# Performance work log

Hardware: AMD Instinct MI355X
Metric: run time of the kernel (lower is better)

## Reference

```python
import jax, jax.numpy as jnp
import numpy as np

D_MODEL = 1024
EXPANSION = 4
NUM_TILES = 4
D_FF = D_MODEL * EXPANSION


def setup_inputs() -> dict:
    key = jax.random.key(0)
    k1, k2, k3, k4, k5 = jax.random.split(key, 5)
    x = jax.random.normal(k1, (8, 2048, D_MODEL), dtype=jnp.float32)
    w_up = jax.random.normal(k2, (D_FF, D_MODEL), dtype=jnp.float32) * 0.02
    b_up = jax.random.normal(k3, (D_FF,), dtype=jnp.float32) * 0.02
    w_down = jax.random.normal(k4, (D_MODEL, D_FF), dtype=jnp.float32) * 0.02
    b_down = jax.random.normal(k5, (D_MODEL,), dtype=jnp.float32) * 0.02
    return {"x": x, "w_up": w_up, "b_up": b_up, "w_down": w_down, "b_down": b_down}


def reference(x, w_up, b_up, w_down, b_down):
    B, T, C = x.shape
    xf = x.reshape(B * T, C)  # [N, d_model]
    N = B * T

    # Emergent tile signatures: sign of per-tile row sums of up_proj weight.
    tile_up = D_FF // NUM_TILES
    signatures = jnp.sign(w_up.reshape(NUM_TILES, tile_up, C).sum(axis=1))  # [num_tiles, d_model]

    # Routing: argmax over input-signature alignment -> one-hot gate.
    scores = xf @ signatures.T                      # [N, num_tiles]
    winner = jnp.argmax(scores, axis=-1)            # [N]
    gate = jax.nn.one_hot(winner, NUM_TILES, dtype=xf.dtype)  # [N, num_tiles]

    # Tile-gated up projection (gate scales output tile blocks), then ReLU.
    hidden = xf @ w_up.T + b_up                     # [N, d_ff]
    hidden = (hidden.reshape(N, NUM_TILES, tile_up) * gate[:, :, None]).reshape(N, D_FF)
    hidden = jax.nn.relu(hidden)

    # Tile-gated down projection.
    tile_down = D_MODEL // NUM_TILES
    out = hidden @ w_down.T + b_down                # [N, d_model]
    out = (out.reshape(N, NUM_TILES, tile_down) * gate[:, :, None]).reshape(N, D_MODEL)

    return out.reshape(B, T, D_MODEL), gate.reshape(B, T, NUM_TILES)
```

## Files before the change

kernel.cpp:

```cpp
#include <hip/hip_runtime.h>
#include <stdint.h>
#include <stddef.h>

#define N_TOK 16384
#define DM    1024
#define DFF   4096
#define NT    4
#define TU    1024
#define TD    256

typedef __attribute__((ext_vector_type(8))) short  short8;
typedef __attribute__((ext_vector_type(4))) short  short4v;
typedef __attribute__((ext_vector_type(4))) float  floatx4;

__device__ inline unsigned short f2bf(float f){
  union { float f; uint32_t u; } v; v.f = f;
  uint32_t u = v.u + 0x7FFFu + ((v.u >> 16) & 1u);
  return (unsigned short)(u >> 16);
}

__device__ __forceinline__ void gll16(const void* g, void* l){
  __builtin_amdgcn_global_load_lds(
      (const __attribute__((address_space(1))) unsigned int*)g,
      (__attribute__((address_space(3))) unsigned int*)l,
      16, 0, 0);
}

__global__ void k_sig_partial(const float* __restrict__ w_up,
                              float* __restrict__ partial,
                              unsigned short* __restrict__ wupb){
  const int b = blockIdx.x, tid = threadIdx.x;
  const int tile = b >> 6, chunk = b & 63;
  const int c0 = tid * 4;
  const int row0 = tile*TU + chunk*16;
  float s0=0.f, s1=0.f, s2=0.f, s3=0.f;
  const float* base = w_up + (size_t)row0 * DM + c0;
  #pragma unroll
  for (int r = 0; r < 16; ++r){
    floatx4 v = *(const floatx4*)(base + (size_t)r * DM);
    s0 += v[0]; s1 += v[1]; s2 += v[2]; s3 += v[3];
    short4v p;
    p[0]=(short)f2bf(v[0]); p[1]=(short)f2bf(v[1]);
    p[2]=(short)f2bf(v[2]); p[3]=(short)f2bf(v[3]);
    *(short4v*)(wupb + (size_t)(row0 + r) * DM + c0) = p;
  }
  float* p = partial + ((size_t)tile*DM + c0) * 64 + chunk;
  p[0] = s0; p[64] = s1; p[128] = s2; p[192] = s3;
}

__global__ void k_sig_final(const float* __restrict__ partial,
                            float* __restrict__ sig){
  const int g = blockIdx.x * 256 + threadIdx.x;
  const float* p = partial + (size_t)g * 64;
  float s = 0.f;
  #pragma unroll
  for (int i = 0; i < 64; ++i) s += p[i];
  sig[g] = (s > 0.f) ? 1.f : ((s < 0.f) ? -1.f : 0.f);
}

__global__ void k_wdown_conv(const float* __restrict__ w,
                             unsigned short* __restrict__ wb){
  const size_t i = ((size_t)blockIdx.x * 256 + threadIdx.x) * 8;
  floatx4 v0 = *(const floatx4*)(w + i);
  floatx4 v1 = *(const floatx4*)(w + i + 4);
  short8 p;
  p[0]=(short)f2bf(v0[0]); p[1]=(short)f2bf(v0[1]); p[2]=(short)f2bf(v0[2]); p[3]=(short)f2bf(v0[3]);
  p[4]=(short)f2bf(v1[0]); p[5]=(short)f2bf(v1[1]); p[6]=(short)f2bf(v1[2]); p[7]=(short)f2bf(v1[3]);
  *(short8*)(wb + i) = p;
}

__global__ __launch_bounds__(256) void k_route(
    const float* __restrict__ x, const float* __restrict__ sig,
    float* __restrict__ gate_out, int* __restrict__ winner,
    unsigned short* __restrict__ xbf){
  __shared__ float ssig[NT * DM];
  const int tid = threadIdx.x;
  for (int i = tid; i < NT*DM; i += 256) ssig[i] = sig[i];
  __syncthreads();
  const int wv = tid >> 6, lane = tid & 63;
  const int n = blockIdx.x * 4 + wv;
  const float* xr = x + (size_t)n * DM;
  unsigned short* xb = xbf + (size_t)n * 2048 + 1024;
  double a0=0.0, a1=0.0, a2=0.0, a3=0.0;
  #pragma unroll
  for (int j = 0; j < 4; ++j){
    const int c = j*256 + lane*4;
    floatx4 v = *(const floatx4*)(xr + c);
    short4v p;
    p[0]=(short)f2bf(v[0]); p[1]=(short)f2bf(v[1]);
    p[2]=(short)f2bf(v[2]); p[3]=(short)f2bf(v[3]);
    *(short4v*)(xb + c) = p;
    #pragma unroll
    for (int u = 0; u < 4; ++u){
      double xv = (double)v[u];
      a0 += xv * (double)ssig[c+u];
      a1 += xv * (double)ssig[DM   + c+u];
      a2 += xv * (double)ssig[2*DM + c+u];
      a3 += xv * (double)ssig[3*DM + c+u];
    }
  }
  #pragma unroll
  for (int off = 32; off > 0; off >>= 1){
    a0 += __shfl_down(a0, off, 64);
    a1 += __shfl_down(a1, off, 64);
    a2 += __shfl_down(a2, off, 64);
    a3 += __shfl_down(a3, off, 64);
  }
  if (lane == 0){
    double s[4] = {a0, a1, a2, a3};
    int w = 0;
    #pragma unroll
    for (int t = 1; t < 4; ++t) if (s[t] > s[w]) w = t;
    floatx4 g = { w==0 ? 1.f:0.f, w==1 ? 1.f:0.f, w==2 ? 1.f:0.f, w==3 ? 1.f:0.f };
    *(floatx4*)(gate_out + (size_t)n * 4) = g;
    winner[n] = w;
  }
}

__global__ void k_hist(const int* __restrict__ winner,
                       int* __restrict__ blk_cnt){
  __shared__ int wcnt[4][NT];
  const int tid = threadIdx.x, wv = tid >> 6, lane = tid & 63;
  const int w = winner[blockIdx.x * 256 + tid];
  #pragma unroll
  for (int t = 0; t < NT; ++t){
    unsigned long long m = __ballot(w == t);
    if (lane == 0) wcnt[wv][t] = __popcll(m);
  }
  __syncthreads();
  if (tid < NT){
    int s = wcnt[0][tid] + wcnt[1][tid] + wcnt[2][tid] + wcnt[3][tid];
    blk_cnt[blockIdx.x * NT + tid] = s;
  }
}

__global__ void k_scan(const int* __restrict__ blk_cnt,
                       int* __restrict__ meta, int* __restrict__ blk_base){
  __shared__ int s[256];
  const int tid = threadIdx.x;
  s[tid] = blk_cnt[tid];
  __syncthreads();
  if (tid == 0){
    int tot[NT] = {0,0,0,0};
    for (int b = 0; b < 64; ++b)
      for (int t = 0; t < NT; ++t) tot[t] += s[b*NT + t];
    int off = 0, base[NT];
    for (int t = 0; t < NT; ++t){ meta[t] = tot[t]; meta[4+t] = off; base[t] = off; off += tot[t]; }
    for (int b = 0; b < 64; ++b)
      for (int t = 0; t < NT; ++t){ int c = s[b*NT + t]; s[b*NT + t] = base[t]; base[t] += c; }
  }
  __syncthreads();
  blk_base[tid] = s[tid];
}

__global__ void k_scatter(const int* __restrict__ winner,
                          const int* __restrict__ blk_base,
                          int* __restrict__ idx){
  __shared__ int wcnt[4][NT];
  const int tid = threadIdx.x, wv = tid >> 6, lane = tid & 63;
  const int n = blockIdx.x * 256 + tid;
  const int w = winner[n];
  unsigned long long mymask = 0;
  #pragma unroll
  for (int t = 0; t < NT; ++t){
    unsigned long long m = __ballot(w == t);
    if (lane == 0) wcnt[wv][t] = __popcll(m);
    if (t == w) mymask = m;
  }
  __syncthreads();
  const unsigned long long below = (lane == 0) ? 0ull : (~0ull >> (64 - lane));
  int pos = blk_base[blockIdx.x * NT + w] + __popcll(mymask & below);
  for (int v = 0; v < wv; ++v) pos += wcnt[v][w];
  idx[pos] = n;
}

__global__ __launch_bounds__(256, 2) void k_gemm1(
    const unsigned short* __restrict__ xbf,
    const unsigned short* __restrict__ wupb,
    const float* __restrict__ b_up, const int* __restrict__ meta,
    const int* __restrict__ idx, unsigned short* __restrict__ hid){
  const int tile = blockIdx.z;
  const int cnt  = meta[tile];
  const int p0   = blockIdx.x * 128;
  if (p0 >= cnt) return;
  const int off  = meta[4 + tile];
  const int nb   = blockIdx.y;

  __shared__ unsigned short smem[16384];
  unsigned short* As0 = smem;
  unsigned short* As1 = smem + 4096;
  unsigned short* Bs0 = smem + 8192;
  unsigned short* Bs1 = smem + 12288;
  __shared__ int nrow[128];

  const int tid = threadIdx.x;
  if (tid < 128){
    int p = p0 + tid;
    nrow[tid] = idx[off + (p < cnt ? p : cnt - 1)];
  }
  __syncthreads();

  const int wv = tid >> 6, lane = tid & 63;
  const int wm = (wv >> 1) * 64, wn = (wv & 1) * 64;
  const int l16 = lane & 15, quad = lane >> 4;

  const int rsub = lane >> 2;
  const int kus  = (lane & 3) * 8;

  const int ra = wv*32 + rsub;
  const unsigned short* aptr0 = xbf + (size_t)nrow[ra]      * 2048 + 1024 + kus;
  const unsigned short* aptr1 = xbf + (size_t)nrow[ra + 16] * 2048 + 1024 + kus;
  const unsigned short* bptr0 = wupb + (size_t)(tile*TU + nb*128 + wv*32 + rsub) * DM + kus;
  const unsigned short* bptr1 = bptr0 + 16 * DM;

  unsigned short* a0d0 = As0 + (wv*32) * 32;  unsigned short* a0d1 = a0d0 + 16*32;
  unsigned short* a1d0 = As1 + (wv*32) * 32;  unsigned short* a1d1 = a1d0 + 16*32;
  unsigned short* b0d0 = Bs0 + (wv*32) * 32;  unsigned short* b0d1 = b0d0 + 16*32;
  unsigned short* b1d0 = Bs1 + (wv*32) * 32;  unsigned short* b1d1 = b1d0 + 16*32;

  floatx4 acc[4][4];
  #pragma unroll
  for (int i = 0; i < 4; ++i)
    #pragma unroll
    for (int j = 0; j < 4; ++j) acc[i][j] = (floatx4){0.f,0.f,0.f,0.f};

  for (int k0 = 0; k0 < DM; k0 += 64){
    gll16(aptr0 + k0,      a0d0);
    gll16(aptr1 + k0,      a0d1);
    gll16(aptr0 + k0 + 32, a1d0);
    gll16(aptr1 + k0 + 32, a1d1);
    gll16(bptr0 + k0,      b0d0);
    gll16(bptr1 + k0,      b0d1);
    gll16(bptr0 + k0 + 32, b1d0);
    gll16(bptr1 + k0 + 32, b1d1);
    __syncthreads();
    {
      short8 af[4], bfr[4];
      #pragma unroll
      for (int i = 0; i < 4; ++i) af[i]  = *(const short8*)(As0 + (wm + i*16 + l16)*32 + quad*8);
      #pragma unroll
      for (int j = 0; j < 4; ++j) bfr[j] = *(const short8*)(Bs0 + (wn + j*16 + l16)*32 + quad*8);
      #pragma unroll
      for (int i = 0; i < 4; ++i)
        #pragma unroll
        for (int j = 0; j < 4; ++j)
          acc[i][j] = __builtin_amdgcn_mfma_f32_16x16x32_bf16(af[i], bfr[j], acc[i][j], 0, 0, 0);
    }
    {
      short8 af[4], bfr[4];
      #pragma unroll
      for (int i = 0; i < 4; ++i) af[i]  = *(const short8*)(As1 + (wm + i*16 + l16)*32 + quad*8);
      #pragma unroll
      for (int j = 0; j < 4; ++j) bfr[j] = *(const short8*)(Bs1 + (wn + j*16 + l16)*32 + quad*8);
      #pragma unroll
      for (int i = 0; i < 4; ++i)
        #pragma unroll
        for (int j = 0; j < 4; ++j)
          acc[i][j] = __builtin_amdgcn_mfma_f32_16x16x32_bf16(af[i], bfr[j], acc[i][j], 0, 0, 0);
    }
    __syncthreads();
  }

  const int gcol0 = nb*128;
  #pragma unroll
  for (int half = 0; half < 2; ++half){
    if ((wv >> 1) == half){
      #pragma unroll
      for (int i = 0; i < 4; ++i){
        #pragma unroll
        for (int j = 0; j < 4; ++j){
          const int col = wn + j*16 + l16;
          const float bias = b_up[tile*TU + gcol0 + col];
          #pragma unroll
          for (int r = 0; r < 4; ++r){
            const int lrow = i*16 + quad*4 + r;
            float v = acc[i][j][r] + bias;
            smem[lrow*136 + col] = f2bf(v > 0.f ? v : 0.f);
          }
        }
      }
    }
    __syncthreads();
    #pragma unroll
    for (int c = tid; c < 1024; c += 256){
      const int lrow = c >> 4, k8 = (c & 15) * 8;
      const int m = half*64 + lrow;
      if (p0 + m < cnt){
        short8 vv = *(const short8*)(smem + lrow*136 + k8);
        *(short8*)(hid + (size_t)nrow[m]*2048 + gcol0 + k8) = vv;
      }
    }
    __syncthreads();
  }
}

__global__ __launch_bounds__(256, 2) void k_gemm2(
    const unsigned short* __restrict__ hid,
    const unsigned short* __restrict__ wdownb,
    const float* __restrict__ b_down, const int* __restrict__ meta,
    const int* __restrict__ idx, float* __restrict__ out){
  const int tile = blockIdx.z;
  const int cnt  = meta[tile];
  const int p0   = blockIdx.x * 32;
  if (p0 >= cnt) return;
  const int off  = meta[4 + tile];

  __shared__ unsigned short smem[18432];
  unsigned short* As0 = smem;
  unsigned short* As1 = smem + 1024;
  unsigned short* Bs0 = smem + 2048;
  unsigned short* Bs1 = smem + 10240;
  float* epi = (float*)smem;
  __shared__ int nrow[32];

  const int tid = threadIdx.x;
  if (tid < 32){
    int p = p0 + tid;
    nrow[tid] = idx[off + (p < cnt ? p : cnt - 1)];
  }
  __syncthreads();

  const int wv = tid >> 6, lane = tid & 63;
  const int wn = wv * 64;
  const int l16 = lane & 15, quad = lane >> 4;

  const int rsub = lane >> 2;
  const int kus  = (lane & 3) * 8;

  const int arow = (wv & 1)*16 + rsub;
  const unsigned short* aptr = hid + (size_t)nrow[arow] * 2048 + kus;
  const int aoff = (wv >> 1) * 32;
  unsigned short* asd = (wv < 2 ? As0 : As1) + ((wv & 1)*16) * 32;
  const unsigned short* bptr = wdownb + (size_t)(tile*TD + wv*64 + rsub) * DFF + tile*TU + kus;
  unsigned short* bsd0 = Bs0 + (wv*64) * 32;
  unsigned short* bsd1 = Bs1 + (wv*64) * 32;

  floatx4 acc[2][4];
  #pragma unroll
  for (int i = 0; i < 2; ++i)
    #pragma unroll
    for (int j = 0; j < 4; ++j) acc[i][j] = (floatx4){0.f,0.f,0.f,0.f};

  for (int k0 = 0; k0 < TU; k0 += 64){
    gll16(aptr + k0 + aoff, asd);
    gll16(bptr + k0,               bsd0);
    gll16(bptr + k0 + 16*DFF,      bsd0 + 16*32);
    gll16(bptr + k0 + 32*DFF,      bsd0 + 32*32);
    gll16(bptr + k0 + 48*DFF,      bsd0 + 48*32);
    gll16(bptr + k0 + 32,          bsd1);
    gll16(bptr + k0 + 32 + 16*DFF, bsd1 + 16*32);
    gll16(bptr + k0 + 32 + 32*DFF, bsd1 + 32*32);
    gll16(bptr + k0 + 32 + 48*DFF, bsd1 + 48*32);
    __syncthreads();
    {
      short8 af[2], bfr[4];
      #pragma unroll
      for (int i = 0; i < 2; ++i) af[i]  = *(const short8*)(As0 + (i*16 + l16)*32 + quad*8);
      #pragma unroll
      for (int j = 0; j < 4; ++j) bfr[j] = *(const short8*)(Bs0 + (wn + j*16 + l16)*32 + quad*8);
      #pragma unroll
      for (int i = 0; i < 2; ++i)
        #pragma unroll
        for (int j = 0; j < 4; ++j)
          acc[i][j] = __builtin_amdgcn_mfma_f32_16x16x32_bf16(af[i], bfr[j], acc[i][j], 0, 0, 0);
    }
    {
      short8 af[2], bfr[4];
      #pragma unroll
      for (int i = 0; i < 2; ++i) af[i]  = *(const short8*)(As1 + (i*16 + l16)*32 + quad*8);
      #pragma unroll
      for (int j = 0; j < 4; ++j) bfr[j] = *(const short8*)(Bs1 + (wn + j*16 + l16)*32 + quad*8);
      #pragma unroll
      for (int i = 0; i < 2; ++i)
        #pragma unroll
        for (int j = 0; j < 4; ++j)
          acc[i][j] = __builtin_amdgcn_mfma_f32_16x16x32_bf16(af[i], bfr[j], acc[i][j], 0, 0, 0);
    }
    __syncthreads();
  }

  const floatx4 z4 = {0.f, 0.f, 0.f, 0.f};
  #pragma unroll
  for (int cb = 0; cb < 4; ++cb){
    if (cb == tile) continue;
    for (int c = tid; c < 32*64; c += 256){
      const int rowl = c >> 6, c4 = (c & 63) * 4;
      if (p0 + rowl < cnt)
        *(floatx4*)(out + (size_t)nrow[rowl]*DM + cb*256 + c4) = z4;
    }
  }

  #pragma unroll
  for (int half = 0; half < 2; ++half){
    #pragma unroll
    for (int j = 0; j < 4; ++j){
      const int col = wn + j*16 + l16;
      const float bias = b_down[tile*TD + col];
      #pragma unroll
      for (int r = 0; r < 4; ++r){
        const int lrow = quad*4 + r;
        epi[lrow*260 + col] = acc[half][j][r] + bias;
      }
    }
    __syncthreads();
    #pragma unroll
    for (int c = tid; c < 1024; c += 256){
      const int lrow = c >> 6, c4 = (c & 63) * 4;
      const int m = half*16 + lrow;
      if (p0 + m < cnt){
        floatx4 v = *(const floatx4*)(epi + lrow*260 + c4);
        *(floatx4*)(out + (size_t)nrow[m]*DM + tile*TD + c4) = v;
      }
    }
    __syncthreads();
  }
}

extern "C" void kernel_launch(void* const* d_in, const int* in_sizes, int n_in,
                              void* d_out, int out_size, void* d_ws, size_t ws_size,
                              hipStream_t stream){
  const float* x      = (const float*)d_in[0];
  const float* w_up   = (const float*)d_in[1];
  const float* b_up   = (const float*)d_in[2];
  const float* w_down = (const float*)d_in[3];
  const float* b_down = (const float*)d_in[4];

  unsigned short* wupb   = (unsigned short*)d_ws;
  unsigned short* wdownb = wupb + (size_t)DFF * DM;
  float* partial = (float*)(wdownb + (size_t)DM * DFF);
  float* sig     = partial + 262144;
  int*   ints    = (int*)(sig + 4096);
  int*   winner   = ints;
  int*   idx      = ints + 16384;
  int*   meta     = ints + 32768;
  int*   blk_cnt  = ints + 32776;
  int*   blk_base = ints + 33032;

  float*          out  = (float*)d_out;
  float*          gate = out + (size_t)N_TOK * DM;
  unsigned short* ob16 = (unsigned short*)d_out;

  k_sig_partial<<<dim3(NT*64), 256, 0, stream>>>(w_up, partial, wupb);
  k_sig_final  <<<dim3(16),    256, 0, stream>>>(partial, sig);
  k_wdown_conv <<<dim3(2048),  256, 0, stream>>>(w_down, wdownb);
  k_route      <<<dim3(N_TOK/4), 256, 0, stream>>>(x, sig, gate, winner, ob16);
  k_hist       <<<dim3(64),    256, 0, stream>>>(winner, blk_cnt);
  k_scan       <<<dim3(1),     256, 0, stream>>>(blk_cnt, meta, blk_base);
  k_scatter    <<<dim3(64),    256, 0, stream>>>(winner, blk_base, idx);
  k_gemm1      <<<dim3(128, 8, NT), 256, 0, stream>>>(ob16, wupb, b_up, meta, idx, ob16);
  k_gemm2      <<<dim3(512, 1, NT), 256, 0, stream>>>(ob16, wdownb, b_down, meta, idx, out);
}
```

Measured before the change: 273.5 us.

## Merge weight-conversion kernels, amortize signature loads in routing, swizzle gemm1 blocks

Merges the w_up signature/conversion kernel and the w_down bf16 conversion into one launch, removing a kernel launch and the gap between them. The routing kernel now handles 16 tokens per block and keeps the signature values in registers, so shared-memory signature reloads are amortized over four tokens per wave. The gemm1 block index is remapped so that consecutive blocks share the same row tile across the eight column blocks, which should improve L2 reuse of the gathered activations. Costs: higher register pressure in routing and fewer routing blocks.

Measured after the change: 267.1 us. -2.3%, faster.

```diff
diff --git a/kernel.cpp b/kernel.cpp
--- a/kernel.cpp
+++ b/kernel.cpp
@@ -26,10 +26,23 @@
       16, 0, 0);
 }
 
-__global__ void k_sig_partial(const float* __restrict__ w_up,
-                              float* __restrict__ partial,
-                              unsigned short* __restrict__ wupb){
-  const int b = blockIdx.x, tid = threadIdx.x;
+__global__ void k_prep(const float* __restrict__ w_up,
+                       const float* __restrict__ w_down,
+                       float* __restrict__ partial,
+                       unsigned short* __restrict__ wupb,
+                       unsigned short* __restrict__ wdownb){
+  const int tid = threadIdx.x;
+  if (blockIdx.x >= 256){
+    const size_t i = ((size_t)(blockIdx.x - 256) * 256 + tid) * 8;
+    floatx4 v0 = *(const floatx4*)(w_down + i);
+    floatx4 v1 = *(const floatx4*)(w_down + i + 4);
+    short8 p;
+    p[0]=(short)f2bf(v0[0]); p[1]=(short)f2bf(v0[1]); p[2]=(short)f2bf(v0[2]); p[3]=(short)f2bf(v0[3]);
+    p[4]=(short)f2bf(v1[0]); p[5]=(short)f2bf(v1[1]); p[6]=(short)f2bf(v1[2]); p[7]=(short)f2bf(v1[3]);
+    *(short8*)(wdownb + i) = p;
+    return;
+  }
+  const int b = blockIdx.x;
   const int tile = b >> 6, chunk = b & 63;
   const int c0 = tid * 4;
   const int row0 = tile*TU + chunk*16;
@@ -58,17 +71,6 @@
   sig[g] = (s > 0.f) ? 1.f : ((s < 0.f) ? -1.f : 0.f);
 }
 
-__global__ void k_wdown_conv(const float* __restrict__ w,
-                             unsigned short* __restrict__ wb){
-  const size_t i = ((size_t)blockIdx.x * 256 + threadIdx.x) * 8;
-  floatx4 v0 = *(const floatx4*)(w + i);
-  floatx4 v1 = *(const floatx4*)(w + i + 4);
-  short8 p;
-  p[0]=(short)f2bf(v0[0]); p[1]=(short)f2bf(v0[1]); p[2]=(short)f2bf(v0[2]); p[3]=(short)f2bf(v0[3]);
-  p[4]=(short)f2bf(v1[0]); p[5]=(short)f2bf(v1[1]); p[6]=(short)f2bf(v1[2]); p[7]=(short)f2bf(v1[3]);
-  *(short8*)(wb + i) = p;
-}
-
 __global__ __launch_bounds__(256) void k_route(
     const float* __restrict__ x, const float* __restrict__ sig,
     float* __restrict__ gate_out, int* __restrict__ winner,
@@ -78,42 +80,55 @@
   for (int i = tid; i < NT*DM; i += 256) ssig[i] = sig[i];
   __syncthreads();
   const int wv = tid >> 6, lane = tid & 63;
-  const int n = blockIdx.x * 4 + wv;
-  const float* xr = x + (size_t)n * DM;
-  unsigned short* xb = xbf + (size_t)n * 2048 + 1024;
-  double a0=0.0, a1=0.0, a2=0.0, a3=0.0;
+
+  floatx4 sg[4][4];
   #pragma unroll
   for (int j = 0; j < 4; ++j){
     const int c = j*256 + lane*4;
-    floatx4 v = *(const floatx4*)(xr + c);
-    short4v p;
-    p[0]=(short)f2bf(v[0]); p[1]=(short)f2bf(v[1]);
-    p[2]=(short)f2bf(v[2]); p[3]=(short)f2bf(v[3]);
-    *(short4v*)(xb + c) = p;
-    #pragma unroll
-    for (int u = 0; u < 4; ++u){
-      double xv = (double)v[u];
-      a0 += xv * (double)ssig[c+u];
-      a1 += xv * (double)ssig[DM   + c+u];
-      a2 += xv * (double)ssig[2*DM + c+u];
-      a3 += xv * (double)ssig[3*DM + c+u];
-    }
-  }
-  #pragma unroll
-  for (int off = 32; off > 0; off >>= 1){
-    a0 += __shfl_down(a0, off, 64);
-    a1 += __shfl_down(a1, off, 64);
-    a2 += __shfl_down(a2, off, 64);
-    a3 += __shfl_down(a3, off, 64);
-  }
-  if (lane == 0){
-    double s[4] = {a0, a1, a2, a3};
-    int w = 0;
-    #pragma unroll
-    for (int t = 1; t < 4; ++t) if (s[t] > s[w]) w = t;
-    floatx4 g = { w==0 ? 1.f:0.f, w==1 ? 1.f:0.f, w==2 ? 1.f:0.f, w==3 ? 1.f:0.f };
-    *(floatx4*)(gate_out + (size_t)n * 4) = g;
-    winner[n] = w;
+    #pragma unroll
+    for (int tt = 0; tt < 4; ++tt)
+      sg[j][tt] = *(const floatx4*)(ssig + tt*DM + c);
+  }
+
+  #pragma unroll
+  for (int t = 0; t < 4; ++t){
+    const int n = blockIdx.x * 16 + wv * 4 + t;
+    const float* xr = x + (size_t)n * DM;
+    unsigned short* xb = xbf + (size_t)n * 2048 + 1024;
+    double a0=0.0, a1=0.0, a2=0.0, a3=0.0;
+    #pragma unroll
+    for (int j = 0; j < 4; ++j){
+      const int c = j*256 + lane*4;
+      floatx4 v = *(const floatx4*)(xr + c);
+      short4v p;
+      p[0]=(short)f2bf(v[0]); p[1]=(short)f2bf(v[1]);
+      p[2]=(short)f2bf(v[2]); p[3]=(short)f2bf(v[3]);
+      *(short4v*)(xb + c) = p;
+      #pragma unroll
+      for (int u = 0; u < 4; ++u){
+        double xv = (double)v[u];
+        a0 += xv * (double)sg[j][0][u];
+        a1 += xv * (double)sg[j][1][u];
+        a2 += xv * (double)sg[j][2][u];
+        a3 += xv * (double)sg[j][3][u];
+      }
+    }
+    #pragma unroll
+    for (int off = 32; off > 0; off >>= 1){
+      a0 += __shfl_down(a0, off, 64);
+      a1 += __shfl_down(a1, off, 64);
+      a2 += __shfl_down(a2, off, 64);
+      a3 += __shfl_down(a3, off, 64);
+    }
+    if (lane == 0){
+      double s[4] = {a0, a1, a2, a3};
+      int w = 0;
+      #pragma unroll
+      for (int tt = 1; tt < 4; ++tt) if (s[tt] > s[w]) w = tt;
+      floatx4 g = { w==0 ? 1.f:0.f, w==1 ? 1.f:0.f, w==2 ? 1.f:0.f, w==3 ? 1.f:0.f };
+      *(floatx4*)(gate_out + (size_t)n * 4) = g;
+      winner[n] = w;
+    }
   }
 }
 
@@ -179,12 +194,15 @@
     const unsigned short* __restrict__ wupb,
     const float* __restrict__ b_up, const int* __restrict__ meta,
     const int* __restrict__ idx, unsigned short* __restrict__ hid){
-  const int tile = blockIdx.z;
+  const int lin  = blockIdx.x + 128*(blockIdx.y + 8*blockIdx.z);
+  const int nb   = (lin >> 3) & 7;
+  const int g    = ((lin >> 6) << 3) | (lin & 7);
+  const int tile = g >> 7;
+  const int p0   = (g & 127) * 128;
+
   const int cnt  = meta[tile];
-  const int p0   = blockIdx.x * 128;
   if (p0 >= cnt) return;
   const int off  = meta[4 + tile];
-  const int nb   = blockIdx.y;
 
   __shared__ unsigned short smem[16384];
   unsigned short* As0 = smem;
@@ -440,13 +458,12 @@
   float*          gate = out + (size_t)N_TOK * DM;
   unsigned short* ob16 = (unsigned short*)d_out;
 
-  k_sig_partial<<<dim3(NT*64), 256, 0, stream>>>(w_up, partial, wupb);
-  k_sig_final  <<<dim3(16),    256, 0, stream>>>(partial, sig);
-  k_wdown_conv <<<dim3(2048),  256, 0, stream>>>(w_down, wdownb);
-  k_route      <<<dim3(N_TOK/4), 256, 0, stream>>>(x, sig, gate, winner, ob16);
-  k_hist       <<<dim3(64),    256, 0, stream>>>(winner, blk_cnt);
-  k_scan       <<<dim3(1),     256, 0, stream>>>(blk_cnt, meta, blk_base);
-  k_scatter    <<<dim3(64),    256, 0, stream>>>(winner, blk_base, idx);
-  k_gemm1      <<<dim3(128, 8, NT), 256, 0, stream>>>(ob16, wupb, b_up, meta, idx, ob16);
-  k_gemm2      <<<dim3(512, 1, NT), 256, 0, stream>>>(ob16, wdownb, b_down, meta, idx, out);
-}
+  k_prep      <<<dim3(2304), 256, 0, stream>>>(w_up, w_down, partial, wupb, wdownb);
+  k_sig_final <<<dim3(16),   256, 0, stream>>>(partial, sig);
+  k_route     <<<dim3(N_TOK/16), 256, 0, stream>>>(x, sig, gate, winner, ob16);
+  k_hist      <<<dim3(64),   256, 0, stream>>>(winner, blk_cnt);
+  k_scan      <<<dim3(1),    256, 0, stream>>>(blk_cnt, meta, blk_base);
+  k_scatter   <<<dim3(64),   256, 0, stream>>>(winner, blk_base, idx);
+  k_gemm1     <<<dim3(128, 8, NT), 256, 0, stream>>>(ob16, wupb, b_up, meta, idx, ob16);
+  k_gemm2     <<<dim3(512, 1, NT), 256, 0, stream>>>(ob16, wdownb, b_down, meta, idx, out);
+}
```
